# Optimization experiments

Hardware: AMD Instinct MI355X
Metric: run time of the kernel (lower is better)

Reference implementation:

```python
import jax, jax.numpy as jnp
import numpy as np

B, T, D = 8, 4096, 128
NUM_CB, K = 8, 1024


def setup_inputs() -> dict:
    key = jax.random.key(0)
    k1, k2 = jax.random.split(key)
    embeddings = jax.random.normal(k1, (B, T, D), dtype=jnp.float32)
    # nn.init.uniform_(w, -1/codebook_size, 1/codebook_size)
    codebooks = jax.random.uniform(k2, (NUM_CB, K, D), dtype=jnp.float32,
                                   minval=-1.0 / K, maxval=1.0 / K)
    return {"embeddings": embeddings, "codebooks": codebooks}


def reference(embeddings, codebooks):
    """Residual VQ: returns (codes [B,T,C] int32, quantized [B,T,D], commitment_loss scalar)."""
    Bv, Tv, Dv = embeddings.shape
    flat = embeddings.reshape(-1, Dv)  # [N, D]

    def step(carry, cb_w):  # cb_w: [K, D]
        residual, quant, loss = carry
        # squared euclidean distance; argmin identical to torch.cdist argmin
        d2 = (jnp.sum(residual * residual, axis=-1, keepdims=True)
              - 2.0 * (residual @ cb_w.T)
              + jnp.sum(cb_w * cb_w, axis=-1))  # [N, K]
        idx = jnp.argmin(d2, axis=-1)  # [N]
        ql = cb_w[idx]  # [N, D] gather
        loss = loss + jnp.mean((jax.lax.stop_gradient(residual) - ql) ** 2)
        quant = quant + ql
        residual = residual - jax.lax.stop_gradient(ql)
        return (residual, quant, loss), idx

    init = (flat, jnp.zeros_like(flat), jnp.float32(0.0))
    (_, quant, loss), codes = jax.lax.scan(step, init, codebooks)
    codes = codes.T.reshape(Bv, Tv, codebooks.shape[0])  # [C,N] -> [B,T,C]
    quant = quant.reshape(Bv, Tv, Dv)
    # straight-through estimator
    quantized = embeddings + jax.lax.stop_gradient(quant - embeddings)
    return codes, quantized, loss / codebooks.shape[0]
```

## Files before the change

kernel.cpp:

```cpp
#include <hip/hip_runtime.h>


#define N_ROWS 32768
#define DIM    128
#define KCB    1024
#define NCB    8
#define MB     128
#define PC     256
#define NPASS  (KCB / PC)
#define KH     64
#define NCHUNK (DIM / KH)
#define LDA    132
#define LDB    68

__global__ __launch_bounds__(256) void zero_ws_kernel(double* lws) {
    if (threadIdx.x < NCB) lws[threadIdx.x] = 0.0;
}

__global__ __launch_bounds__(256) void c2_kernel(const float* __restrict__ cbw,
                                                 float* __restrict__ c2g) {
#pragma clang fp contract(off)
    int code = blockIdx.x * 256 + threadIdx.x;
    const float* row = cbw + (size_t)code * DIM;
    float s[8];
    for (int j = 0; j < 8; ++j) { float x = row[j]; s[j] = x * x; }
    for (int m = 1; m < 16; ++m)
        for (int j = 0; j < 8; ++j) { float x = row[m * 8 + j]; float p = x * x; s[j] += p; }
    c2g[code] = ((s[0] + s[1]) + (s[2] + s[3])) + ((s[4] + s[5]) + (s[6] + s[7]));
}

__global__ __launch_bounds__(512, 1) void rvq_kernel(
    const float* __restrict__ emb, const float* __restrict__ cbw,
    const float* __restrict__ c2g, float* __restrict__ out,
    double* __restrict__ lws)
{
    __shared__ __align__(16) float a_lds[MB * LDA];
    __shared__ __align__(16) float b_lds[PC * LDB];
    __shared__ float r2_lds[MB];
    __shared__ float c2_lds[PC];
    __shared__ float scr[4 * MB];
    __shared__ float minv_lds[MB];
    __shared__ int   mini_lds[MB];
    __shared__ int   codes_lds[NCB * MB];

    const int tid  = threadIdx.x;
    const int tcol = tid & 31;
    const int half = (tid >> 5) & 1;
    const int trow = tid >> 6;
    const size_t base = (size_t)blockIdx.x * MB;

#pragma unroll
    for (int s = 0; s < 8; ++s) {
        int f4 = s * 512 + tid;
        int r = f4 >> 5, k4 = f4 & 31;
        float4 v = *(const float4*)(emb + (base + r) * DIM + (size_t)k4 * 4);
        *(float4*)(a_lds + r * LDA + k4 * 4) = v;
    }
    __syncthreads();

    {
#pragma clang fp contract(off)
        int r = tid & 127, q = tid >> 7;
        float x0 = a_lds[r * LDA + 2 * q];     float s0 = x0 * x0;
        float x1 = a_lds[r * LDA + 2 * q + 1]; float s1 = x1 * x1;
        for (int m = 1; m < 16; ++m) {
            float y0 = a_lds[r * LDA + m * 8 + 2 * q];     float p0 = y0 * y0; s0 += p0;
            float y1 = a_lds[r * LDA + m * 8 + 2 * q + 1]; float p1 = y1 * y1; s1 += p1;
        }
        scr[q * MB + r] = s0 + s1;
    }
    __syncthreads();
    if (tid < MB) {
#pragma clang fp contract(off)
        float t0 = scr[tid], t1 = scr[MB + tid], t2 = scr[2 * MB + tid], t3 = scr[3 * MB + tid];
        r2_lds[tid] = (t0 + t1) + (t2 + t3);
    }

#pragma clang loop unroll(disable)
    for (int cb = 0; cb < NCB; ++cb) {
        const float* cbbase = cbw + (size_t)cb * KCB * DIM;
        if (tid < MB) minv_lds[tid] = 3.4e38f;

#pragma clang loop unroll(disable)
        for (int pass = 0; pass < NPASS; ++pass) {
            float acc[8][8];
#pragma unroll
            for (int i = 0; i < 8; ++i)
#pragma unroll
                for (int j = 0; j < 8; ++j) acc[i][j] = 0.f;

#pragma clang loop unroll(disable)
            for (int chunk = 0; chunk < NCHUNK; ++chunk) {
                __syncthreads();
                const float* bsrc = cbbase + (size_t)pass * PC * DIM + chunk * KH;
#pragma unroll
                for (int s = 0; s < 8; ++s) {
                    int f4 = s * 512 + tid;
                    int c = f4 >> 4, kk = f4 & 15;
                    float4 v = *(const float4*)(bsrc + (size_t)c * DIM + kk * 4);
                    *(float4*)(b_lds + c * LDB + kk * 4) = v;
                }
                if (chunk == 0 && tid < PC) c2_lds[tid] = c2g[cb * KCB + pass * PC + tid];
                __syncthreads();

                const float* abw = a_lds + (trow * 16 + half * 8) * LDA + chunk * KH;
                const float* bvb = b_lds + tcol * LDB;
#pragma unroll
                for (int k4 = 0; k4 < 16; ++k4) {
                    float4 bv[8];
#pragma unroll
                    for (int j = 0; j < 8; ++j)
                        bv[j] = *(const float4*)(bvb + j * 32 * LDB + k4 * 4);
#pragma unroll
                    for (int i = 0; i < 8; ++i) {
                        float4 av = *(const float4*)(abw + i * LDA + k4 * 4);
#pragma unroll
                        for (int j = 0; j < 8; ++j) {
                            acc[i][j] = fmaf(av.x, bv[j].x, acc[i][j]);
                            acc[i][j] = fmaf(av.y, bv[j].y, acc[i][j]);
                            acc[i][j] = fmaf(av.z, bv[j].z, acc[i][j]);
                            acc[i][j] = fmaf(av.w, bv[j].w, acc[i][j]);
                        }
                    }
                }
            }

            {
#pragma clang fp contract(off)
                float c2v[8];
#pragma unroll
                for (int j = 0; j < 8; ++j) c2v[j] = c2_lds[tcol + 32 * j];
#pragma unroll
                for (int i = 0; i < 8; ++i) {
                    int rr = trow * 16 + half * 8 + i;
                    float r2v = r2_lds[rr];
                    float v = 3.4e38f; int ix = 0;
#pragma unroll
                    for (int j = 0; j < 8; ++j) {
                        float t  = r2v - 2.0f * acc[i][j];
                        float d2 = t + c2v[j];
                        int   cg = pass * PC + tcol + 32 * j;
                        if (d2 < v) { v = d2; ix = cg; }
                    }
#pragma unroll
                    for (int m = 1; m <= 16; m <<= 1) {
                        float v2 = __shfl_xor(v, m, 64);
                        int  ix2 = __shfl_xor(ix, m, 64);
                        if (v2 < v || (v2 == v && ix2 < ix)) { v = v2; ix = ix2; }
                    }
                    if (tcol == 0) {
                        if (v < minv_lds[rr]) { minv_lds[rr] = v; mini_lds[rr] = ix; }
                    }
                }
            }
        }
        __syncthreads();

        {
#pragma clang fp contract(off)
            int r = tid & 127, q = tid >> 7;
            int widx = mini_lds[r];
            if (q == 0) codes_lds[cb * MB + r] = widx;
            const float* ql = cbbase + (size_t)widx * DIM;
            float s0 = 0.f, s1 = 0.f;
            double lacc = 0.0;
            for (int m = 0; m < 16; ++m) {
                int k0 = m * 8 + 2 * q;
                float a0 = a_lds[r * LDA + k0];
                float q0 = ql[k0];
                float n0 = a0 - q0;
                a_lds[r * LDA + k0] = n0;
                float p0 = n0 * n0;
                if (m == 0) s0 = p0; else s0 += p0;
                lacc += (double)p0;
                int k1 = k0 + 1;
                float a1 = a_lds[r * LDA + k1];
                float q1 = ql[k1];
                float n1 = a1 - q1;
                a_lds[r * LDA + k1] = n1;
                float p1 = n1 * n1;
                if (m == 0) s1 = p1; else s1 += p1;
                lacc += (double)p1;
            }
            scr[q * MB + r] = s0 + s1;
            for (int off = 32; off > 0; off >>= 1) lacc += __shfl_down(lacc, off, 64);
            if ((tid & 63) == 0) atomicAdd(&lws[cb], lacc);
        }
        __syncthreads();
        if (tid < MB) {
#pragma clang fp contract(off)
            float t0 = scr[tid], t1 = scr[MB + tid], t2 = scr[2 * MB + tid], t3 = scr[3 * MB + tid];
            r2_lds[tid] = (t0 + t1) + (t2 + t3);
        }
    }
    __syncthreads();

    if (tid < MB) {
        int r = tid;
        float4 u, v;
        u.x = (float)codes_lds[0 * MB + r]; u.y = (float)codes_lds[1 * MB + r];
        u.z = (float)codes_lds[2 * MB + r]; u.w = (float)codes_lds[3 * MB + r];
        v.x = (float)codes_lds[4 * MB + r]; v.y = (float)codes_lds[5 * MB + r];
        v.z = (float)codes_lds[6 * MB + r]; v.w = (float)codes_lds[7 * MB + r];
        *(float4*)(out + (base + r) * NCB)     = u;
        *(float4*)(out + (base + r) * NCB + 4) = v;
    }

    {
#pragma clang fp contract(off)
        int r = tid >> 2, q4 = tid & 3;
        size_t rg = base + r;
        int cds[NCB];
#pragma unroll
        for (int cb = 0; cb < NCB; ++cb) cds[cb] = codes_lds[cb * MB + r];
        float* qout = out + (size_t)N_ROWS * NCB;
#pragma unroll
        for (int ii = 0; ii < 8; ++ii) {
            int k = q4 * 32 + ii * 4;
            float4 qv = make_float4(0.f, 0.f, 0.f, 0.f);
#pragma unroll
            for (int cb = 0; cb < NCB; ++cb) {
                float4 cv = *(const float4*)(cbw + ((size_t)cb * KCB + cds[cb]) * DIM + k);
                qv.x += cv.x; qv.y += cv.y; qv.z += cv.z; qv.w += cv.w;
            }
            float4 ev = *(const float4*)(emb + rg * DIM + k);
            float4 ov;
            ov.x = ev.x + (qv.x - ev.x);
            ov.y = ev.y + (qv.y - ev.y);
            ov.z = ev.z + (qv.z - ev.z);
            ov.w = ev.w + (qv.w - ev.w);
            *(float4*)(qout + rg * DIM + k) = ov;
        }
    }
}

__global__ __launch_bounds__(64) void finish_loss_kernel(const double* __restrict__ lws,
                                                         float* __restrict__ out_loss) {
    if (threadIdx.x == 0 && blockIdx.x == 0) {
        float l = 0.f;
        for (int cb = 0; cb < NCB; ++cb) {
            float m = (float)(lws[cb] / 4194304.0);
            l = l + m;
        }
        out_loss[0] = l / 8.0f;
    }
}

extern "C" void kernel_launch(void* const* d_in, const int* in_sizes, int n_in,
                              void* d_out, int out_size, void* d_ws, size_t ws_size,
                              hipStream_t stream) {
    const float* emb = (const float*)d_in[0];
    const float* cbw = (const float*)d_in[1];
    float* out = (float*)d_out;
    double* lws = (double*)d_ws;
    float* c2g = (float*)((char*)d_ws + 256);

    hipLaunchKernelGGL(zero_ws_kernel, dim3(1), dim3(64), 0, stream, lws);
    hipLaunchKernelGGL(c2_kernel, dim3(32), dim3(256), 0, stream, cbw, c2g);
    hipLaunchKernelGGL(rvq_kernel, dim3(256), dim3(512), 0, stream, emb, cbw, c2g, out, lws);
    hipLaunchKernelGGL(finish_loss_kernel, dim3(1), dim3(64), 0, stream, lws,
                       out + (size_t)N_ROWS * NCB + (size_t)N_ROWS * DIM);
}
```

Measured before the change: 1.166 ms.

## Broadcast A rows via readlane and stage codebook tiles with direct global-to-LDS loads

Reshapes the per-thread distance tile from 8x8 to 16 rows by 4 codes. Each wave now owns 16 rows, and A values are broadcast across lanes with readlane instead of being loaded from LDS per thread. Codebook tiles are copied straight from global memory into a k-major LDS layout using global_load_lds, and launch bounds now allow two blocks per CU. The aim is to cut LDS read traffic, VGPR pressure and staging instructions, at the cost of many scalar readlane operations and a wider 64-lane shuffle reduction.

New measurement: 1.787 ms. +53.3%, slower.

```diff
diff --git a/kernel.cpp b/kernel.cpp
--- a/kernel.cpp
+++ b/kernel.cpp
@@ -11,7 +11,13 @@
 #define KH     64
 #define NCHUNK (DIM / KH)
 #define LDA    132
-#define LDB    68
+
+typedef __attribute__((address_space(1))) const void GLOBv;
+typedef __attribute__((address_space(3))) void LDSv;
+
+__device__ __forceinline__ float rdlane(float v, int l) {
+    return __builtin_bit_cast(float, __builtin_amdgcn_readlane(__builtin_bit_cast(int, v), l));
+}
 
 __global__ __launch_bounds__(256) void zero_ws_kernel(double* lws) {
     if (threadIdx.x < NCB) lws[threadIdx.x] = 0.0;
@@ -29,13 +35,13 @@
     c2g[code] = ((s[0] + s[1]) + (s[2] + s[3])) + ((s[4] + s[5]) + (s[6] + s[7]));
 }
 
-__global__ __launch_bounds__(512, 1) void rvq_kernel(
+__global__ __launch_bounds__(512, 2) void rvq_kernel(
     const float* __restrict__ emb, const float* __restrict__ cbw,
     const float* __restrict__ c2g, float* __restrict__ out,
     double* __restrict__ lws)
 {
     __shared__ __align__(16) float a_lds[MB * LDA];
-    __shared__ __align__(16) float b_lds[PC * LDB];
+    __shared__ float4 b_lds4[16 * PC];
     __shared__ float r2_lds[MB];
     __shared__ float c2_lds[PC];
     __shared__ float scr[4 * MB];
@@ -44,8 +50,7 @@
     __shared__ int   codes_lds[NCB * MB];
 
     const int tid  = threadIdx.x;
-    const int tcol = tid & 31;
-    const int half = (tid >> 5) & 1;
+    const int tcol = tid & 63;
     const int trow = tid >> 6;
     const size_t base = (size_t)blockIdx.x * MB;
 
@@ -83,43 +88,49 @@
 
 #pragma clang loop unroll(disable)
         for (int pass = 0; pass < NPASS; ++pass) {
-            float acc[8][8];
-#pragma unroll
-            for (int i = 0; i < 8; ++i)
-#pragma unroll
-                for (int j = 0; j < 8; ++j) acc[i][j] = 0.f;
+            float acc[16][4];
+#pragma unroll
+            for (int i = 0; i < 16; ++i)
+#pragma unroll
+                for (int j = 0; j < 4; ++j) acc[i][j] = 0.f;
 
 #pragma clang loop unroll(disable)
             for (int chunk = 0; chunk < NCHUNK; ++chunk) {
                 __syncthreads();
-                const float* bsrc = cbbase + (size_t)pass * PC * DIM + chunk * KH;
-#pragma unroll
-                for (int s = 0; s < 8; ++s) {
-                    int f4 = s * 512 + tid;
-                    int c = f4 >> 4, kk = f4 & 15;
-                    float4 v = *(const float4*)(bsrc + (size_t)c * DIM + kk * 4);
-                    *(float4*)(b_lds + c * LDB + kk * 4) = v;
+                {
+                    const float* bsrc = cbbase + (size_t)pass * PC * DIM + chunk * KH;
+#pragma unroll
+                    for (int s = 0; s < 8; ++s) {
+                        int combo = s * 8 + trow;
+                        int kk = combo >> 2, cg = combo & 3;
+                        const float* g = bsrc + (size_t)(cg * 64 + tcol) * DIM + kk * 4;
+                        float4* l = b_lds4 + kk * PC + cg * 64;
+                        __builtin_amdgcn_global_load_lds((GLOBv*)g, (LDSv*)l, 16, 0, 0);
+                    }
                 }
                 if (chunk == 0 && tid < PC) c2_lds[tid] = c2g[cb * KCB + pass * PC + tid];
                 __syncthreads();
 
-                const float* abw = a_lds + (trow * 16 + half * 8) * LDA + chunk * KH;
-                const float* bvb = b_lds + tcol * LDB;
-#pragma unroll
-                for (int k4 = 0; k4 < 16; ++k4) {
-                    float4 bv[8];
-#pragma unroll
-                    for (int j = 0; j < 8; ++j)
-                        bv[j] = *(const float4*)(bvb + j * 32 * LDB + k4 * 4);
-#pragma unroll
-                    for (int i = 0; i < 8; ++i) {
-                        float4 av = *(const float4*)(abw + i * LDA + k4 * 4);
-#pragma unroll
-                        for (int j = 0; j < 8; ++j) {
-                            acc[i][j] = fmaf(av.x, bv[j].x, acc[i][j]);
-                            acc[i][j] = fmaf(av.y, bv[j].y, acc[i][j]);
-                            acc[i][j] = fmaf(av.z, bv[j].z, acc[i][j]);
-                            acc[i][j] = fmaf(av.w, bv[j].w, acc[i][j]);
+                const float* agat = a_lds + (trow * 16 + (tid & 15)) * LDA + chunk * KH;
+#pragma unroll
+                for (int kk = 0; kk < 16; ++kk) {
+                    float4 gq = *(const float4*)(agat + kk * 4);
+                    float4 bv[4];
+#pragma unroll
+                    for (int j = 0; j < 4; ++j)
+                        bv[j] = b_lds4[kk * PC + tcol + 64 * j];
+#pragma unroll
+                    for (int i = 0; i < 16; ++i) {
+                        float a0 = rdlane(gq.x, i);
+                        float a1 = rdlane(gq.y, i);
+                        float a2 = rdlane(gq.z, i);
+                        float a3 = rdlane(gq.w, i);
+#pragma unroll
+                        for (int j = 0; j < 4; ++j) {
+                            acc[i][j] = fmaf(a0, bv[j].x, acc[i][j]);
+                            acc[i][j] = fmaf(a1, bv[j].y, acc[i][j]);
+                            acc[i][j] = fmaf(a2, bv[j].z, acc[i][j]);
+                            acc[i][j] = fmaf(a3, bv[j].w, acc[i][j]);
                         }
                     }
                 }
@@ -127,23 +138,23 @@
 
             {
 #pragma clang fp contract(off)
-                float c2v[8];
-#pragma unroll
-                for (int j = 0; j < 8; ++j) c2v[j] = c2_lds[tcol + 32 * j];
-#pragma unroll
-                for (int i = 0; i < 8; ++i) {
-                    int rr = trow * 16 + half * 8 + i;
+                float c2v[4];
+#pragma unroll
+                for (int j = 0; j < 4; ++j) c2v[j] = c2_lds[tcol + 64 * j];
+#pragma unroll
+                for (int i = 0; i < 16; ++i) {
+                    int rr = trow * 16 + i;
                     float r2v = r2_lds[rr];
                     float v = 3.4e38f; int ix = 0;
 #pragma unroll
-                    for (int j = 0; j < 8; ++j) {
+                    for (int j = 0; j < 4; ++j) {
                         float t  = r2v - 2.0f * acc[i][j];
                         float d2 = t + c2v[j];
-                        int   cg = pass * PC + tcol + 32 * j;
+                        int   cg = pass * PC + tcol + 64 * j;
                         if (d2 < v) { v = d2; ix = cg; }
                     }
 #pragma unroll
-                    for (int m = 1; m <= 16; m <<= 1) {
+                    for (int m = 1; m <= 32; m <<= 1) {
                         float v2 = __shfl_xor(v, m, 64);
                         int  ix2 = __shfl_xor(ix, m, 64);
                         if (v2 < v || (v2 == v && ix2 < ix)) { v = v2; ix = ix2; }
```
